# Kernel tuning notes

Hardware: AMD Instinct MI355X
Metric: run time of the kernel (lower is better)

The kernel has to match this reference:

```python
import jax, jax.numpy as jnp
import numpy as np

B, L, D, E = 64, 256, 2048, 1024
WIN = 3
NEG = -1e18


def setup_inputs() -> dict:
    key = jax.random.key(0)
    ks = jax.random.split(key, 8)
    clip_ft = jax.random.normal(ks[0], (B, L, D), dtype=jnp.float32)
    clip_lens = jax.random.randint(ks[1], (B,), 3, L + 1).astype(jnp.int32)
    s = 1.0 / np.sqrt(D)
    w_mot_wei = jax.random.uniform(ks[2], (D,), minval=-s, maxval=s)
    b_mot_wei = jnp.zeros((), jnp.float32)
    w_mot_fc = jax.random.uniform(ks[3], (D, E), minval=-s, maxval=s)
    b_mot_fc = jnp.zeros((E,), jnp.float32)
    w_app_fc = jax.random.uniform(ks[4], (D, E), minval=-s, maxval=s)
    b_app_fc = jnp.zeros((E,), jnp.float32)
    se = 1.0 / np.sqrt(E)
    w_pool = jax.random.uniform(ks[5], (E,), minval=-se, maxval=se)
    b_pool = jnp.zeros((), jnp.float32)
    return {"clip_ft": clip_ft, "clip_lens": clip_lens,
            "w_mot_wei": w_mot_wei, "b_mot_wei": b_mot_wei,
            "w_mot_fc": w_mot_fc, "b_mot_fc": b_mot_fc,
            "w_app_fc": w_app_fc, "b_app_fc": b_app_fc,
            "w_pool": w_pool, "b_pool": b_pool}


def _gelu(x):
    return jax.nn.gelu(x, approximate=False)  # torch nn.GELU default (erf)


def reference(clip_ft, clip_lens, w_mot_wei, b_mot_wei, w_mot_fc, b_mot_fc,
              w_app_fc, b_app_fc, w_pool, b_pool):
    b, l, d = clip_ft.shape
    pos = jnp.arange(l)
    pad = pos[None, :] >= clip_lens[:, None]                      # True = pad
    mot_scores = clip_ft @ w_mot_wei + b_mot_wei                  # (B, L)
    attn_scores = jnp.where(pad, NEG, mot_scores)
    # sliding window of size 3 (vectorized replacement of the python loop)
    lw = l - WIN + 1                                              # L - 2
    win_ft = jnp.stack([clip_ft[:, i:i + lw] for i in range(WIN)], axis=2)   # (B, L-2, 3, D)
    win_sc = jnp.stack([attn_scores[:, i:i + lw] for i in range(WIN)], axis=2)  # (B, L-2, 3)
    a = jax.nn.softmax(win_sc, axis=2)
    vid_clip = jnp.einsum('blw,blwd->bld', a, win_ft)             # (B, L-2, D)
    motion = _gelu(vid_clip @ w_mot_fc + b_mot_fc)                # (B, L-2, E)
    appearance = _gelu(clip_ft @ w_app_fc + b_app_fc)             # (B, L, E)
    # masked-softmax attention pooling (motion uses lens-2, appearance uses lens)
    s_mot = _gelu(motion @ w_pool + b_pool)                       # (B, L-2)
    pad_mot = jnp.arange(lw)[None, :] >= (clip_lens - 2)[:, None]
    a_mot = jax.nn.softmax(jnp.where(pad_mot, NEG, s_mot), axis=1)
    mot_pooled = jnp.einsum('bl,ble->be', a_mot, motion)          # (B, E)
    s_app = _gelu(appearance @ w_pool + b_pool)                   # (B, L)
    a_app = jax.nn.softmax(jnp.where(pad, NEG, s_app), axis=1)
    app_pooled = jnp.einsum('bl,ble->be', a_app, appearance)      # (B, E)
    return jnp.concatenate([mot_pooled, app_pooled], axis=-1)     # (B, 2E)
```

## Files before the change

### kernel.cpp

```cpp
#include <hip/hip_runtime.h>
#include <cstdint>

#define NEGF (-1e18f)
#define GK 2048
#define GN 1024

typedef __attribute__((ext_vector_type(8))) short short8;
typedef __attribute__((ext_vector_type(4))) float f32x4;
typedef __attribute__((ext_vector_type(4))) unsigned short us4;
typedef __attribute__((ext_vector_type(8))) unsigned short us8;

__device__ __forceinline__ unsigned short f2bf(float f) {
    unsigned int u = __float_as_uint(f);
    u += 0x7FFFu + ((u >> 16) & 1u);
    return (unsigned short)(u >> 16);
}
__device__ __forceinline__ float bf2f(unsigned short h) {
    return __uint_as_float(((unsigned int)h) << 16);
}
__device__ __forceinline__ float gelu_erf(float x) {
    return 0.5f * x * (1.0f + erff(x * 0.70710678118654752f));
}
__device__ __forceinline__ float gelu_fast(float x) {
    const float y = 1.5957691216057308f * (x + 0.044715f * x * x * x);
    const float t = 1.0f - 2.0f / (__expf(y) + 1.0f);
    return 0.5f * x * (1.0f + t);
}
__device__ __forceinline__ void async_copy16(const void* g, void* l) {
    __builtin_amdgcn_global_load_lds(
        (const __attribute__((address_space(1))) unsigned int*)g,
        (__attribute__((address_space(3))) unsigned int*)l,
        16, 0, 0);
}

__global__ __launch_bounds__(256) void wtrans2_kernel(const float* __restrict__ wmot,
                                                      const float* __restrict__ wapp,
                                                      const int* __restrict__ lens,
                                                      unsigned short* __restrict__ wmotT,
                                                      unsigned short* __restrict__ wappT,
                                                      int* __restrict__ bases) {
    if (blockIdx.x == 2048) {
        const int lane = threadIdx.x;
        if (lane < 64) {
            const int L = lens[lane];
            int sm_ = L - 2, sa_ = L;
            const int vm = sm_, va = sa_;
            #pragma unroll
            for (int off = 1; off < 64; off <<= 1) {
                const int tm = __shfl_up(sm_, off);
                const int ta = __shfl_up(sa_, off);
                if (lane >= off) { sm_ += tm; sa_ += ta; }
            }
            bases[lane] = sm_ - vm;
            bases[65 + lane] = sa_ - va;
            if (lane == 63) { bases[64] = sm_; bases[129] = sa_; }
        }
        return;
    }
    const int which = blockIdx.x >> 10;
    const float* w = which ? wapp : wmot;
    unsigned short* wT = which ? wappT : wmotT;
    const int idx = (blockIdx.x & 1023) * 256 + threadIdx.x;
    const int n = idx & 1023;
    const int k0 = (idx >> 10) << 3;
    us8 o;
    #pragma unroll
    for (int j = 0; j < 8; ++j) o[j] = f2bf(w[(size_t)(k0 + j) * 1024 + n]);
    *(us8*)(wT + (size_t)n * 2048 + k0) = o;
}

__global__ __launch_bounds__(256) void prep2_kernel(const float* __restrict__ clip_ft,
                                                    const int* __restrict__ lens,
                                                    const int* __restrict__ bases,
                                                    const float* __restrict__ w_mot_wei,
                                                    const float* __restrict__ bsc,
                                                    unsigned short* __restrict__ app,
                                                    unsigned short* __restrict__ vid) {
    __shared__ float sm2[2][4];
    const int b = blockIdx.x >> 3;
    const int c = blockIdx.x & 7;
    const int len = lens[b];
    const int l0 = c * 32;
    if (l0 >= len) return;
    const int bm = bases[b], ba = bases[65 + b];
    const int t = threadIdx.x;
    const int lane = t & 63, wv = t >> 6;
    const int d0 = t * 8;
    const float bias = bsc[0];
    const float* base = clip_ft + ((size_t)b * 256) * 2048 + d0;
    float wm[8];
    {
        f32x4 u = *(const f32x4*)(w_mot_wei + d0);
        f32x4 v = *(const f32x4*)(w_mot_wei + d0 + 4);
        #pragma unroll
        for (int j = 0; j < 4; ++j) { wm[j] = u[j]; wm[4 + j] = v[j]; }
    }
    float x0[8], x1[8], cur[8];
    float sc0 = NEGF, sc1 = NEGF, sc2 = NEGF;
    for (int i = 0; i < 34; ++i) {
        const int l = l0 + i;
        const bool live = (l < len);
        if (live) {
            const f32x4* p = (const f32x4*)(base + (size_t)l * 2048);
            f32x4 u = p[0], v = p[1];
            #pragma unroll
            for (int j = 0; j < 4; ++j) { cur[j] = u[j]; cur[4 + j] = v[j]; }
            if (i < 32) {
                us8 o;
                #pragma unroll
                for (int j = 0; j < 8; ++j) o[j] = f2bf(cur[j]);
                *(us8*)(app + ((size_t)(ba + l)) * 2048 + d0) = o;
            }
            float p8 = cur[0]*wm[0] + cur[1]*wm[1] + cur[2]*wm[2] + cur[3]*wm[3]
                     + cur[4]*wm[4] + cur[5]*wm[5] + cur[6]*wm[6] + cur[7]*wm[7];
            #pragma unroll
            for (int off = 32; off; off >>= 1) p8 += __shfl_xor(p8, off);
            if (lane == 0) sm2[i & 1][wv] = p8;
        }
        __syncthreads();
        sc2 = live ? (sm2[i & 1][0] + sm2[i & 1][1]) + (sm2[i & 1][2] + sm2[i & 1][3]) + bias
                   : NEGF;
        if (i >= 2) {
            const int lw = l - 2;
            if (lw < len - 2) {
                const float mx = fmaxf(sc0, fmaxf(sc1, sc2));
                const float e0 = expf(sc0 - mx), e1 = expf(sc1 - mx), e2 = expf(sc2 - mx);
                const float inv = 1.0f / (e0 + e1 + e2);
                const float a0 = e0 * inv, a1 = e1 * inv, a2 = e2 * inv;
                us8 o;
                #pragma unroll
                for (int j = 0; j < 8; ++j) o[j] = f2bf(a0 * x0[j] + a1 * x1[j] + a2 * cur[j]);
                *(us8*)(vid + ((size_t)(bm + lw)) * 2048 + d0) = o;
            }
        }
        #pragma unroll
        for (int j = 0; j < 8; ++j) { x0[j] = x1[j]; x1[j] = cur[j]; }
        sc0 = sc1; sc1 = sc2;
    }
}

__global__ __launch_bounds__(512, 4) void gemm3q_kernel(
        const unsigned short* __restrict__ Avid, const unsigned short* __restrict__ Aapp,
        const unsigned short* __restrict__ Bmot, const unsigned short* __restrict__ Bapp,
        const float* __restrict__ bmot, const float* __restrict__ bapp,
        const float* __restrict__ w_pool, const int* __restrict__ bases,
        unsigned short* __restrict__ Cmot, unsigned short* __restrict__ Capp,
        float* __restrict__ pspart) {
    __shared__ __align__(16) unsigned short lds_[3 * 12288];
    const int bid = blockIdx.x;
    const int virt = (bid & 7) * 128 + (bid >> 3);
    const int which = virt >> 9;
    const int rem = virt & 511;
    const int ntile = rem & 3;
    const int mt_idx = rem >> 2;
    const int mtile = (mt_idx & 31) * 4 + (mt_idx >> 5);
    const int row0 = mtile * 128, col0 = ntile * 256;
    const int total = bases[which ? 129 : 64];
    if (row0 >= total) return;
    const unsigned short* A  = which ? Aapp : Avid;
    const unsigned short* Bt = which ? Bapp : Bmot;
    const float* bias        = which ? bapp : bmot;
    unsigned short* C        = which ? Capp : Cmot;
    const int t = threadIdx.x, lane = t & 63, wave = t >> 6;
    const int wm = wave >> 2, wn = wave & 3;
    const int lr = lane & 15, sl = lane >> 4;

    const int srow = t >> 2;
    const int sk16 = (t & 3) ^ ((srow >> 1) & 3);
    const unsigned short* gA  = A  + (size_t)(row0 + srow) * GK + sk16 * 8;
    const unsigned short* gB0 = Bt + (size_t)(col0 + srow) * GK + sk16 * 8;
    const unsigned short* gB1 = Bt + (size_t)(col0 + srow + 128) * GK + sk16 * 8;
    const int wbase = wave << 9;

#define STAGE(d, kt) do { \
    async_copy16(gA  + (kt) * 32, lds_ + (d) * 12288 +        wbase); \
    async_copy16(gB0 + (kt) * 32, lds_ + (d) * 12288 + 4096 + wbase); \
    async_copy16(gB1 + (kt) * 32, lds_ + (d) * 12288 + 8192 + wbase); } while (0)

#define KSTEP(CUR) do { \
    const unsigned short* lb = lds_ + (CUR) * 12288; \
    short8 aF[4], bF[4]; \
    _Pragma("unroll") \
    for (int m = 0; m < 4; ++m) { \
        const int r = wm * 64 + m * 16 + lr; \
        aF[m] = *(const short8*)(lb + r * 32 + ((sl ^ ((r >> 1) & 3)) << 3)); \
    } \
    _Pragma("unroll") \
    for (int n = 0; n < 4; ++n) { \
        const int cc = wn * 64 + n * 16 + lr; \
        bF[n] = *(const short8*)(lb + 4096 + cc * 32 + ((sl ^ ((cc >> 1) & 3)) << 3)); \
    } \
    _Pragma("unroll") \
    for (int m = 0; m < 4; ++m) \
        _Pragma("unroll") \
        for (int n = 0; n < 4; ++n) \
            acc[m][n] = __builtin_amdgcn_mfma_f32_16x16x32_bf16(aF[m], bF[n], acc[m][n], 0, 0, 0); \
    } while (0)

    f32x4 acc[4][4] = {};
    STAGE(0, 0);
    STAGE(1, 1);

    int cur = 0, stg = 2;
    #pragma unroll 3
    for (int kt = 0; kt < 62; ++kt) {
        asm volatile("s_waitcnt vmcnt(3)" ::: "memory");
        __builtin_amdgcn_s_barrier();
        __builtin_amdgcn_sched_barrier(0);
        STAGE(stg, kt + 2);
        KSTEP(cur);
        cur = (cur == 2) ? 0 : cur + 1;
        stg = (stg == 2) ? 0 : stg + 1;
    }
    asm volatile("s_waitcnt vmcnt(3)" ::: "memory");
    __builtin_amdgcn_s_barrier();
    __builtin_amdgcn_sched_barrier(0);
    KSTEP(cur);
    cur = (cur == 2) ? 0 : cur + 1;
    asm volatile("s_waitcnt vmcnt(0)" ::: "memory");
    __builtin_amdgcn_s_barrier();
    __builtin_amdgcn_sched_barrier(0);
    KSTEP(cur);
#undef STAGE
#undef KSTEP

    float wp[4], bz[4];
    #pragma unroll
    for (int n = 0; n < 4; ++n) {
        const int col = col0 + wn * 64 + n * 16 + lr;
        wp[n] = w_pool[col];
        bz[n] = bias[col];
    }
    const int strip = ntile * 4 + wn;
    #pragma unroll
    for (int m = 0; m < 4; ++m) {
        #pragma unroll
        for (int i = 0; i < 4; ++i) {
            const int row = row0 + wm * 64 + m * 16 + sl * 4 + i;
            float pr = 0.f;
            #pragma unroll
            for (int n = 0; n < 4; ++n) {
                const int col = col0 + wn * 64 + n * 16 + lr;
                const float g = gelu_fast(acc[m][n][i] + bz[n]);
                pr += g * wp[n];
                C[(size_t)row * GN + col] = f2bf(g);
            }
            #pragma unroll
            for (int off = 8; off; off >>= 1) pr += __shfl_xor(pr, off);
            if (lr == 0) pspart[((size_t)which * 16384 + row) * 16 + strip] = pr;
        }
    }
}

__global__ __launch_bounds__(256) void pool2_kernel(const unsigned short* __restrict__ motion,
                                                    const unsigned short* __restrict__ appearance,
                                                    const float* __restrict__ pspart,
                                                    const int* __restrict__ lens,
                                                    const int* __restrict__ bases,
                                                    const float* __restrict__ b_pool,
                                                    float* __restrict__ out) {
    __shared__ float sm[256];
    __shared__ float red[8];
    const int which = blockIdx.x & 1;
    const int half = (blockIdx.x >> 1) & 1;
    const int b = blockIdx.x >> 2;
    const int base = which ? bases[65 + b] : bases[b];
    const unsigned short* mat = (which ? appearance : motion) + (size_t)base * 1024;
    const int valid = which ? lens[b] : lens[b] - 2;
    const int t = threadIdx.x, lane = t & 63, wv = t >> 6;
    float v = NEGF;
    if (t < valid) {
        const float* pp = pspart + ((size_t)which * 16384 + base + t) * 16;
        float s = 0.f;
        #pragma unroll
        for (int j = 0; j < 16; ++j) s += pp[j];
        v = gelu_erf(s + b_pool[0]);
    }
    float mx = v;
    #pragma unroll
    for (int off = 32; off; off >>= 1) mx = fmaxf(mx, __shfl_xor(mx, off));
    if (lane == 0) red[wv] = mx;
    __syncthreads();
    mx = fmaxf(fmaxf(red[0], red[1]), fmaxf(red[2], red[3]));
    const float e = expf(v - mx);
    float s = e;
    #pragma unroll
    for (int off = 32; off; off >>= 1) s += __shfl_xor(s, off);
    if (lane == 0) red[4 + wv] = s;
    __syncthreads();
    s = red[4] + red[5] + red[6] + red[7];
    sm[t] = e / s;
    __syncthreads();
    const int col0 = half * 512 + t * 2;
    float a0 = 0.f, a1 = 0.f;
    for (int l = 0; l < valid; ++l) {
        const float al = sm[l];
        const unsigned int hv = *(const unsigned int*)(mat + (size_t)l * 1024 + col0);
        a0 += al * bf2f((unsigned short)(hv & 0xFFFF));
        a1 += al * bf2f((unsigned short)(hv >> 16));
    }
    float* o = out + (size_t)b * 2048 + which * 1024 + col0;
    o[0] = a0; o[1] = a1;
}

extern "C" void kernel_launch(void* const* d_in, const int* in_sizes, int n_in,
                              void* d_out, int out_size, void* d_ws, size_t ws_size,
                              hipStream_t stream) {
    const float* clip_ft   = (const float*)d_in[0];
    const int*   clip_lens = (const int*)d_in[1];
    const float* w_mot_wei = (const float*)d_in[2];
    const float* b_mot_wei = (const float*)d_in[3];
    const float* w_mot_fc  = (const float*)d_in[4];
    const float* b_mot_fc  = (const float*)d_in[5];
    const float* w_app_fc  = (const float*)d_in[6];
    const float* b_app_fc  = (const float*)d_in[7];
    const float* w_pool    = (const float*)d_in[8];
    const float* b_pool    = (const float*)d_in[9];
    float* out = (float*)d_out;

    char* ws = (char*)d_ws;
    size_t off = 0;
    auto carve = [&](size_t bytes) { void* p = ws + off; off += (bytes + 255) & ~(size_t)255; return p; };
    int*            bases  = (int*)carve((size_t)130 * 4);
    float*          pspart = (float*)carve((size_t)2 * 16384 * 16 * 4);
    unsigned short* wmotT  = (unsigned short*)carve((size_t)1024 * 2048 * 2);
    unsigned short* wappT  = (unsigned short*)carve((size_t)1024 * 2048 * 2);
    unsigned short* appb   = (unsigned short*)carve((size_t)64 * 256 * 2048 * 2);
    unsigned short* vidb   = (unsigned short*)carve((size_t)64 * 256 * 2048 * 2);
    unsigned short* motion = (unsigned short*)carve((size_t)64 * 256 * 1024 * 2);
    unsigned short* appear = (unsigned short*)carve((size_t)64 * 256 * 1024 * 2);
    (void)ws_size; (void)in_sizes; (void)n_in; (void)out_size;

    wtrans2_kernel<<<2049, 256, 0, stream>>>(w_mot_fc, w_app_fc, clip_lens,
                                             wmotT, wappT, bases);
    prep2_kernel<<<512, 256, 0, stream>>>(clip_ft, clip_lens, bases, w_mot_wei, b_mot_wei,
                                          appb, vidb);
    gemm3q_kernel<<<1024, 512, 0, stream>>>(vidb, appb, wmotT, wappT,
                                            b_mot_fc, b_app_fc, w_pool, bases,
                                            motion, appear, pspart);
    pool2_kernel<<<256, 256, 0, stream>>>(motion, appear, pspart, clip_lens, bases, b_pool, out);
}
```

Baseline: 158.4 us.

## Fuse weight transpose and prep kernels, recompute prefix bases locally per block

Merges the weight transpose/bf16 conversion kernel and the clip prep kernel into one launch. The prefix-sum offsets are now recomputed inside each block of the prep, GEMM and pool kernels instead of being stored to a global buffer, which removes a launch and the dependency between the two early kernels. The prep loop also prefetches the next row's clip features one iteration ahead to hide load latency. In exchange every block does a small redundant scan and an extra __syncthreads, and the prefetch uses more registers.

```diff
diff --git a/kernel.cpp b/kernel.cpp
--- a/kernel.cpp
+++ b/kernel.cpp
@@ -33,57 +33,50 @@
         16, 0, 0);
 }
 
-__global__ __launch_bounds__(256) void wtrans2_kernel(const float* __restrict__ wmot,
-                                                      const float* __restrict__ wapp,
-                                                      const int* __restrict__ lens,
-                                                      unsigned short* __restrict__ wmotT,
-                                                      unsigned short* __restrict__ wappT,
-                                                      int* __restrict__ bases) {
-    if (blockIdx.x == 2048) {
-        const int lane = threadIdx.x;
-        if (lane < 64) {
-            const int L = lens[lane];
-            int sm_ = L - 2, sa_ = L;
-            const int vm = sm_, va = sa_;
-            #pragma unroll
-            for (int off = 1; off < 64; off <<= 1) {
-                const int tm = __shfl_up(sm_, off);
-                const int ta = __shfl_up(sa_, off);
-                if (lane >= off) { sm_ += tm; sa_ += ta; }
-            }
-            bases[lane] = sm_ - vm;
-            bases[65 + lane] = sa_ - va;
-            if (lane == 63) { bases[64] = sm_; bases[129] = sa_; }
-        }
+__global__ __launch_bounds__(256) void fused1_kernel(const float* __restrict__ wmot,
+                                                     const float* __restrict__ wapp,
+                                                     const float* __restrict__ clip_ft,
+                                                     const int* __restrict__ lens,
+                                                     const float* __restrict__ w_mot_wei,
+                                                     const float* __restrict__ bsc,
+                                                     unsigned short* __restrict__ wmotT,
+                                                     unsigned short* __restrict__ wappT,
+                                                     unsigned short* __restrict__ app,
+                                                     unsigned short* __restrict__ vid) {
+    if (blockIdx.x < 2048) {
+        const int which = blockIdx.x >> 10;
+        const float* w = which ? wapp : wmot;
+        unsigned short* wT = which ? wappT : wmotT;
+        const int idx = (blockIdx.x & 1023) * 256 + threadIdx.x;
+        const int n = idx & 1023;
+        const int k0 = (idx >> 10) << 3;
+        us8 o;
+        #pragma unroll
+        for (int j = 0; j < 8; ++j) o[j] = f2bf(w[(size_t)(k0 + j) * 1024 + n]);
+        *(us8*)(wT + (size_t)n * 2048 + k0) = o;
         return;
     }
-    const int which = blockIdx.x >> 10;
-    const float* w = which ? wapp : wmot;
-    unsigned short* wT = which ? wappT : wmotT;
-    const int idx = (blockIdx.x & 1023) * 256 + threadIdx.x;
-    const int n = idx & 1023;
-    const int k0 = (idx >> 10) << 3;
-    us8 o;
-    #pragma unroll
-    for (int j = 0; j < 8; ++j) o[j] = f2bf(w[(size_t)(k0 + j) * 1024 + n]);
-    *(us8*)(wT + (size_t)n * 2048 + k0) = o;
-}
-
-__global__ __launch_bounds__(256) void prep2_kernel(const float* __restrict__ clip_ft,
-                                                    const int* __restrict__ lens,
-                                                    const int* __restrict__ bases,
-                                                    const float* __restrict__ w_mot_wei,
-                                                    const float* __restrict__ bsc,
-                                                    unsigned short* __restrict__ app,
-                                                    unsigned short* __restrict__ vid) {
     __shared__ float sm2[2][4];
-    const int b = blockIdx.x >> 3;
-    const int c = blockIdx.x & 7;
+    __shared__ int sb2[2];
+    const int bid = blockIdx.x - 2048;
+    const int b = bid >> 3;
+    const int c = bid & 7;
     const int len = lens[b];
     const int l0 = c * 32;
     if (l0 >= len) return;
-    const int bm = bases[b], ba = bases[65 + b];
     const int t = threadIdx.x;
+    if (t < 64) {
+        const int L2 = lens[t];
+        const int m0 = L2 - 2, a0 = L2;
+        int mi = m0, ai = a0;
+        #pragma unroll
+        for (int off = 1; off < 64; off <<= 1) {
+            const int tm = __shfl_up(mi, off);
+            const int ta = __shfl_up(ai, off);
+            if (t >= off) { mi += tm; ai += ta; }
+        }
+        if (t == b) { sb2[0] = mi - m0; sb2[1] = ai - a0; }
+    }
     const int lane = t & 63, wv = t >> 6;
     const int d0 = t * 8;
     const float bias = bsc[0];
@@ -95,16 +88,27 @@
         #pragma unroll
         for (int j = 0; j < 4; ++j) { wm[j] = u[j]; wm[4 + j] = v[j]; }
     }
-    float x0[8], x1[8], cur[8];
+    __syncthreads();
+    const int bm = sb2[0], ba = sb2[1];
+    float x0[8], x1[8], cur[8], nxt[8];
+    {
+        const f32x4* p = (const f32x4*)(base + (size_t)l0 * 2048);
+        f32x4 u = p[0], v = p[1];
+        #pragma unroll
+        for (int j = 0; j < 4; ++j) { cur[j] = u[j]; cur[4 + j] = v[j]; }
+    }
     float sc0 = NEGF, sc1 = NEGF, sc2 = NEGF;
     for (int i = 0; i < 34; ++i) {
         const int l = l0 + i;
         const bool live = (l < len);
-        if (live) {
-            const f32x4* p = (const f32x4*)(base + (size_t)l * 2048);
+        const bool liveN = (i < 33) && (l + 1 < len);
+        if (liveN) {
+            const f32x4* p = (const f32x4*)(base + (size_t)(l + 1) * 2048);
             f32x4 u = p[0], v = p[1];
             #pragma unroll
-            for (int j = 0; j < 4; ++j) { cur[j] = u[j]; cur[4 + j] = v[j]; }
+            for (int j = 0; j < 4; ++j) { nxt[j] = u[j]; nxt[4 + j] = v[j]; }
+        }
+        if (live) {
             if (i < 32) {
                 us8 o;
                 #pragma unroll
@@ -134,7 +138,7 @@
             }
         }
         #pragma unroll
-        for (int j = 0; j < 8; ++j) { x0[j] = x1[j]; x1[j] = cur[j]; }
+        for (int j = 0; j < 8; ++j) { x0[j] = x1[j]; x1[j] = cur[j]; if (liveN) cur[j] = nxt[j]; }
         sc0 = sc1; sc1 = sc2;
     }
 }
@@ -143,10 +147,11 @@
         const unsigned short* __restrict__ Avid, const unsigned short* __restrict__ Aapp,
         const unsigned short* __restrict__ Bmot, const unsigned short* __restrict__ Bapp,
         const float* __restrict__ bmot, const float* __restrict__ bapp,
-        const float* __restrict__ w_pool, const int* __restrict__ bases,
+        const float* __restrict__ w_pool, const int* __restrict__ lens,
         unsigned short* __restrict__ Cmot, unsigned short* __restrict__ Capp,
         float* __restrict__ pspart) {
     __shared__ __align__(16) unsigned short lds_[3 * 12288];
+    __shared__ int stot;
     const int bid = blockIdx.x;
     const int virt = (bid & 7) * 128 + (bid >> 3);
     const int which = virt >> 9;
@@ -155,8 +160,14 @@
     const int mt_idx = rem >> 2;
     const int mtile = (mt_idx & 31) * 4 + (mt_idx >> 5);
     const int row0 = mtile * 128, col0 = ntile * 256;
-    const int total = bases[which ? 129 : 64];
-    if (row0 >= total) return;
+    if (threadIdx.x < 64) {
+        int v = lens[threadIdx.x] - (which ? 0 : 2);
+        #pragma unroll
+        for (int off = 32; off; off >>= 1) v += __shfl_xor(v, off);
+        if (threadIdx.x == 0) stot = v;
+    }
+    __syncthreads();
+    if (row0 >= stot) return;
     const unsigned short* A  = which ? Aapp : Avid;
     const unsigned short* Bt = which ? Bapp : Bmot;
     const float* bias        = which ? bapp : bmot;
@@ -256,18 +267,30 @@
                                                     const unsigned short* __restrict__ appearance,
                                                     const float* __restrict__ pspart,
                                                     const int* __restrict__ lens,
-                                                    const int* __restrict__ bases,
                                                     const float* __restrict__ b_pool,
                                                     float* __restrict__ out) {
     __shared__ float sm[256];
     __shared__ float red[8];
+    __shared__ int sbase;
     const int which = blockIdx.x & 1;
     const int half = (blockIdx.x >> 1) & 1;
     const int b = blockIdx.x >> 2;
-    const int base = which ? bases[65 + b] : bases[b];
+    const int t = threadIdx.x, lane = t & 63, wv = t >> 6;
+    if (t < 64) {
+        const int L2 = lens[t];
+        const int v0 = which ? L2 : L2 - 2;
+        int vi = v0;
+        #pragma unroll
+        for (int off = 1; off < 64; off <<= 1) {
+            const int tv = __shfl_up(vi, off);
+            if (t >= off) vi += tv;
+        }
+        if (t == b) sbase = vi - v0;
+    }
+    const int valid = which ? lens[b] : lens[b] - 2;
+    __syncthreads();
+    const int base = sbase;
     const unsigned short* mat = (which ? appearance : motion) + (size_t)base * 1024;
-    const int valid = which ? lens[b] : lens[b] - 2;
-    const int t = threadIdx.x, lane = t & 63, wv = t >> 6;
     float v = NEGF;
     if (t < valid) {
         const float* pp = pspart + ((size_t)which * 16384 + base + t) * 16;
@@ -321,7 +344,6 @@
     char* ws = (char*)d_ws;
     size_t off = 0;
     auto carve = [&](size_t bytes) { void* p = ws + off; off += (bytes + 255) & ~(size_t)255; return p; };
-    int*            bases  = (int*)carve((size_t)130 * 4);
     float*          pspart = (float*)carve((size_t)2 * 16384 * 16 * 4);
     unsigned short* wmotT  = (unsigned short*)carve((size_t)1024 * 2048 * 2);
     unsigned short* wappT  = (unsigned short*)carve((size_t)1024 * 2048 * 2);
@@ -331,12 +353,10 @@
     unsigned short* appear = (unsigned short*)carve((size_t)64 * 256 * 1024 * 2);
     (void)ws_size; (void)in_sizes; (void)n_in; (void)out_size;
 
-    wtrans2_kernel<<<2049, 256, 0, stream>>>(w_mot_fc, w_app_fc, clip_lens,
-                                             wmotT, wappT, bases);
-    prep2_kernel<<<512, 256, 0, stream>>>(clip_ft, clip_lens, bases, w_mot_wei, b_mot_wei,
-                                          appb, vidb);
+    fused1_kernel<<<2560, 256, 0, stream>>>(w_mot_fc, w_app_fc, clip_ft, clip_lens,
+                                            w_mot_wei, b_mot_wei, wmotT, wappT, appb, vidb);
     gemm3q_kernel<<<1024, 512, 0, stream>>>(vidb, appb, wmotT, wappT,
-                                            b_mot_fc, b_app_fc, w_pool, bases,
+                                            b_mot_fc, b_app_fc, w_pool, clip_lens,
                                             motion, appear, pspart);
-    pool2_kernel<<<256, 256, 0, stream>>>(motion, appear, pspart, clip_lens, bases, b_pool, out);
-}
+    pool2_kernel<<<256, 256, 0, stream>>>(motion, appear, pspart, clip_lens, b_pool, out);
+}
```

Result: faster. 155.1 us (-2.1%).
